# Optimization experiments

Measured on AMD Instinct MI355X. Metric: run time of the kernel, lower is better.

Reference implementation:

```python
import jax, jax.numpy as jnp
import numpy as np

N = 100000      # nodes
E = 1600000     # edges
F_IN = 64       # CFG.feature_dim
H = 128         # CFG.hidden_dim
G = 128         # graphs in batch
LN_EPS = 1e-5


def setup_inputs() -> dict:
    key = jax.random.key(0)
    ks = jax.random.split(key, 12)
    x = jax.random.normal(ks[0], (N, F_IN), dtype=jnp.float32)
    edge_index = jax.random.randint(ks[1], (2, E), 0, N)
    batch = jnp.sort(jax.random.randint(ks[2], (N,), 0, G))
    # GCNConv weights (glorot-ish scale) and biases
    W1 = jax.random.normal(ks[3], (F_IN, H), dtype=jnp.float32) * (1.0 / np.sqrt(F_IN))
    b1 = jnp.zeros((H,), jnp.float32)
    W2 = jax.random.normal(ks[4], (H, H), dtype=jnp.float32) * (1.0 / np.sqrt(H))
    b2 = jnp.zeros((H,), jnp.float32)
    # LayerNorm affine params
    g1 = jnp.ones((H,), jnp.float32)
    beta1 = jnp.zeros((H,), jnp.float32)
    g2 = jnp.ones((H,), jnp.float32)
    beta2 = jnp.zeros((H,), jnp.float32)
    return {"x": x, "edge_index": edge_index, "batch": batch,
            "W1": W1, "b1": b1, "g1": g1, "beta1": beta1,
            "W2": W2, "b2": b2, "g2": g2, "beta2": beta2,
            "num_graphs": G}


def _gcn_conv(h, W, b, src, dst, n):
    """PyG GCNConv: add self-loops, symmetric D^-1/2 (A+I) D^-1/2 (h W) + b."""
    hw = h @ W                                   # [n, out]
    loop = jnp.arange(n, dtype=src.dtype)
    s = jnp.concatenate([src, loop])             # [E+n]
    d = jnp.concatenate([dst, loop])
    deg = jax.ops.segment_sum(jnp.ones_like(s, jnp.float32), d, num_segments=n)
    dinv = jax.lax.rsqrt(jnp.maximum(deg, 1e-12))
    norm = dinv[s] * dinv[d]                     # [E+n]
    msg = hw[s] * norm[:, None]                  # gather + scale
    out = jax.ops.segment_sum(msg, d, num_segments=n)
    return out + b


def _layer_norm(h, gamma, beta):
    mu = jnp.mean(h, axis=-1, keepdims=True)
    var = jnp.mean(jnp.square(h - mu), axis=-1, keepdims=True)
    return (h - mu) * jax.lax.rsqrt(var + LN_EPS) * gamma + beta


def reference(x, edge_index, batch, W1, b1, g1, beta1, W2, b2, g2, beta2, num_graphs):
    src, dst = edge_index[0], edge_index[1]
    n = x.shape[0]
    h = _gcn_conv(x, W1, b1, src, dst, n)
    h = _layer_norm(h, g1, beta1)
    h = jax.nn.relu(h)
    h = _gcn_conv(h, W2, b2, src, dst, n)
    h = _layer_norm(h, g2, beta2)
    # is_inverted defaults to False -> no sign flip
    sums = jax.ops.segment_sum(h, batch, num_segments=num_graphs)      # [G, H]
    counts = jax.ops.segment_sum(jnp.ones((n,), jnp.float32), batch, num_segments=num_graphs)
    return sums / jnp.maximum(counts, 1.0)[:, None]
```

## Files before the change

### kernel.cpp

```cpp
#include <hip/hip_runtime.h>
#include <hip/hip_bf16.h>

#define LN_EPS 1e-5f

typedef __attribute__((ext_vector_type(8))) short short8v;
typedef __attribute__((ext_vector_type(4))) float float4v;

__device__ __forceinline__ float bflo(unsigned u) { return __uint_as_float(u << 16); }
__device__ __forceinline__ float bfhi(unsigned u) { return __uint_as_float(u & 0xffff0000u); }
__device__ __forceinline__ unsigned short f2bf(float f) {
    __hip_bfloat16 b = __float2bfloat16(f);
    return *reinterpret_cast<unsigned short*>(&b);
}
__device__ __forceinline__ unsigned pack2(float x, float y) {
    __hip_bfloat162 t = __float22bfloat162_rn(make_float2(x, y));
    return *reinterpret_cast<unsigned*>(&t);
}
__device__ __forceinline__ void add8(float* a, uint4 u) {
    a[0] += bflo(u.x); a[1] += bfhi(u.x);
    a[2] += bflo(u.y); a[3] += bfhi(u.y);
    a[4] += bflo(u.z); a[5] += bfhi(u.z);
    a[6] += bflo(u.w); a[7] += bfhi(u.w);
}

union U4S8 { uint4 u; short8v s; };


#define CHUNK 4096
#define NBMAX 512
#define BCAP 5120
#define CSRCAP 8192

__launch_bounds__(256)
__global__ void k_bucket(const int* __restrict__ src, const int* __restrict__ dst, int e,
                         int* __restrict__ gcnt, unsigned* __restrict__ stage) {
    __shared__ unsigned ebuf[CHUNK];
    __shared__ unsigned short ebkt[CHUNK];
    __shared__ int hist[NBMAX];
    __shared__ int base[NBMAX];
    int tid = threadIdx.x;
    int c0 = blockIdx.x * CHUNK;
    if (c0 >= e) return;
    int cnt = min(CHUNK, e - c0);

    for (int t = tid; t < NBMAX; t += 256) hist[t] = 0;
    __syncthreads();
    for (int t = tid; t < cnt; t += 256) {
        unsigned s = (unsigned)src[c0 + t];
        unsigned d = (unsigned)dst[c0 + t];
        ebuf[t] = s | ((d & 0xffu) << 24);
        ebkt[t] = (unsigned short)(d >> 8);
        atomicAdd(&hist[d >> 8], 1);
    }
    __syncthreads();
    for (int b = tid; b < NBMAX; b += 256) {
        int h = hist[b];
        if (h > 0) base[b] = b * BCAP + atomicAdd(&gcnt[b], h);
    }
    __syncthreads();
    for (int t = tid; t < cnt; t += 256) {
        int p = atomicAdd(&base[ebkt[t]], 1);
        stage[p] = ebuf[t];
    }
}

__launch_bounds__(256)
__global__ void k_csr(const unsigned* __restrict__ stage, const int* __restrict__ gcnt,
                      int* __restrict__ csr_src, int* __restrict__ row_start,
                      int* __restrict__ row_end, float* __restrict__ dinv,
                      const float* __restrict__ x, unsigned* __restrict__ xb, int n) {
    __shared__ int cntl[256];
    __shared__ int sc[256];
    __shared__ int excl[256];
    __shared__ float dfl[256];
    __shared__ int cbuf[CSRCAP];
    int b = blockIdx.x;
    int lo = b << 8;
    int nn = min(n - lo, 256);
    int tid = threadIdx.x;
    int s0 = b * BCAP;
    int cntB = gcnt[b];

    cntl[tid] = 0;
    __syncthreads();
    for (int t = tid; t < cntB; t += 256) {
        int dl = (int)(stage[s0 + t] >> 24);
        atomicAdd(&cntl[dl], 1);
    }
    __syncthreads();
    int deg = (tid < nn) ? cntl[tid] : 0;
    sc[tid] = deg; __syncthreads();
    for (int o = 1; o < 256; o <<= 1) {
        int t = (tid >= o) ? sc[tid - o] : 0;
        __syncthreads();
        sc[tid] += t;
        __syncthreads();
    }
    excl[tid] = sc[tid] - deg;
    float dv = rsqrtf((float)(deg + 1));
    dfl[tid] = dv;
    if (tid < nn) {
        row_start[lo + tid] = s0 + excl[tid];
        row_end[lo + tid]   = s0 + excl[tid] + deg;
        dinv[lo + tid] = dv;
    }
    cntl[tid] = 0;
    __syncthreads();
    for (int t = tid; t < cntB; t += 256) {
        unsigned ed = stage[s0 + t];
        int dl = (int)(ed >> 24);
        int r = atomicAdd(&cntl[dl], 1);
        int p = excl[dl] + r;
        if (p < CSRCAP) cbuf[p] = (int)(ed & 0x00ffffffu);
        else csr_src[s0 + p] = (int)(ed & 0x00ffffffu);
    }
    __syncthreads();
    int lim = min(cntB, CSRCAP);
    for (int t = tid; t < lim; t += 256) csr_src[s0 + t] = cbuf[t];

    const float4* x4 = (const float4*)x;
    uint2* xb2 = (uint2*)xb;
    for (int idx = tid; idx < nn * 16; idx += 256) {
        int node = idx >> 4, c = idx & 15;
        size_t p = ((size_t)(lo + node) << 4) + c;
        float4 v = x4[p];
        float d = dfl[node];
        xb2[p] = make_uint2(pack2(v.x * d, v.y * d), pack2(v.z * d, v.w * d));
    }
}


__global__ void k_agg64b(const uint4* __restrict__ x4, const float* __restrict__ dinv,
                         const int* __restrict__ row_start, const int* __restrict__ row_end,
                         const int* __restrict__ csr_src, uint4* __restrict__ out4, int n) {
    int lane = threadIdx.x & 63;
    int g = lane >> 3, c = lane & 7;
    int wid = (blockIdx.x * blockDim.x + threadIdx.x) >> 6;
    int nw = (gridDim.x * blockDim.x) >> 6;
    for (int i = wid; i < n; i += nw) {
        float a[8] = {0.f, 0.f, 0.f, 0.f, 0.f, 0.f, 0.f, 0.f};
        if (g == 0) {
            uint4 su = x4[(size_t)i * 8 + c];
            add8(a, su);
        }
        int j0 = row_start[i], j1 = row_end[i];
        int j = j0 + g;
        for (; j + 8 < j1; j += 16) {
            int s0 = csr_src[j], s1 = csr_src[j + 8];
            uint4 u0 = x4[(size_t)s0 * 8 + c];
            uint4 u1 = x4[(size_t)s1 * 8 + c];
            add8(a, u0);
            add8(a, u1);
        }
        if (j < j1) {
            int s0 = csr_src[j];
            uint4 u0 = x4[(size_t)s0 * 8 + c];
            add8(a, u0);
        }
        #pragma unroll
        for (int k = 0; k < 8; ++k) {
            a[k] += __shfl_xor(a[k], 8);
            a[k] += __shfl_xor(a[k], 16);
            a[k] += __shfl_xor(a[k], 32);
        }
        if (g == 0) {
            float di = dinv[i];
            uint4 o;
            o.x = pack2(a[0] * di, a[1] * di);
            o.y = pack2(a[2] * di, a[3] * di);
            o.z = pack2(a[4] * di, a[5] * di);
            o.w = pack2(a[6] * di, a[7] * di);
            out4[(size_t)i * 8 + c] = o;
        }
    }
}

__global__ void k_agg128b(const uint4* __restrict__ h4, const float* __restrict__ dinv,
                          const int* __restrict__ row_start, const int* __restrict__ row_end,
                          const int* __restrict__ csr_src, uint4* __restrict__ out4, int n) {
    int lane = threadIdx.x & 63;
    int q = lane >> 4, c = lane & 15;
    int wid = (blockIdx.x * blockDim.x + threadIdx.x) >> 6;
    int nw = (gridDim.x * blockDim.x) >> 6;
    for (int i = wid; i < n; i += nw) {
        float a[8] = {0.f, 0.f, 0.f, 0.f, 0.f, 0.f, 0.f, 0.f};
        if (q == 0) {
            uint4 su = h4[(size_t)i * 16 + c];
            add8(a, su);
        }
        int j0 = row_start[i], j1 = row_end[i];
        int j = j0 + q;
        for (; j + 12 < j1; j += 16) {
            int s0 = csr_src[j], s1 = csr_src[j + 4];
            int s2 = csr_src[j + 8], s3 = csr_src[j + 12];
            uint4 u0 = h4[(size_t)s0 * 16 + c];
            uint4 u1 = h4[(size_t)s1 * 16 + c];
            uint4 u2 = h4[(size_t)s2 * 16 + c];
            uint4 u3 = h4[(size_t)s3 * 16 + c];
            add8(a, u0);
            add8(a, u1);
            add8(a, u2);
            add8(a, u3);
        }
        for (; j < j1; j += 4) {
            int s0 = csr_src[j];
            uint4 u0 = h4[(size_t)s0 * 16 + c];
            add8(a, u0);
        }
        #pragma unroll
        for (int k = 0; k < 8; ++k) {
            a[k] += __shfl_xor(a[k], 16);
            a[k] += __shfl_xor(a[k], 32);
        }
        if (q == 0) {
            float di = dinv[i];
            uint4 o;
            o.x = pack2(a[0] * di, a[1] * di);
            o.y = pack2(a[2] * di, a[3] * di);
            o.z = pack2(a[4] * di, a[5] * di);
            o.w = pack2(a[6] * di, a[7] * di);
            out4[(size_t)i * 16 + c] = o;
        }
    }
}


__launch_bounds__(256)
__global__ void k_mm1(const unsigned* __restrict__ aggb, const float* __restrict__ W1,
                      const float* __restrict__ b1, const float* __restrict__ g1,
                      const float* __restrict__ be1, const float* __restrict__ dinv,
                      uint4* __restrict__ hb4, int ntiles) {
    int lane = threadIdx.x & 63;
    int wv = threadIdx.x >> 6;
    int wpb = blockDim.x >> 6;
    int lc = lane & 15, lg = lane >> 4;

    short8v B[2][8];
    #pragma unroll
    for (int ks = 0; ks < 2; ++ks)
        #pragma unroll
        for (int cb = 0; cb < 8; ++cb) {
            short8v f;
            #pragma unroll
            for (int j = 0; j < 8; ++j) {
                int k = ks * 32 + lg * 8 + j;
                f[j] = (short)f2bf(W1[k * 128 + cb * 16 + lc]);
            }
            B[ks][cb] = f;
        }
    float bs[8], gm[8], bt[8];
    #pragma unroll
    for (int cb = 0; cb < 8; ++cb) {
        bs[cb] = b1[cb * 16 + lc];
        gm[cb] = g1[cb * 16 + lc];
        bt[cb] = be1[cb * 16 + lc];
    }

    for (int t = blockIdx.x * wpb + wv; t < ntiles; t += gridDim.x * wpb) {
        size_t arow = (size_t)(t * 16 + lc) * 32;
        U4S8 a0, a1;
        a0.u = *(const uint4*)&aggb[arow + lg * 4];
        a1.u = *(const uint4*)&aggb[arow + 16 + lg * 4];
        float4v acc[8];
        #pragma unroll
        for (int cb = 0; cb < 8; ++cb) acc[cb] = (float4v){0.f, 0.f, 0.f, 0.f};
        #pragma unroll
        for (int cb = 0; cb < 8; ++cb) {
            acc[cb] = __builtin_amdgcn_mfma_f32_16x16x32_bf16(a0.s, B[0][cb], acc[cb], 0, 0, 0);
            acc[cb] = __builtin_amdgcn_mfma_f32_16x16x32_bf16(a1.s, B[1][cb], acc[cb], 0, 0, 0);
        }
        #pragma unroll
        for (int reg = 0; reg < 4; ++reg) {
            float s = 0.f, q = 0.f;
            #pragma unroll
            for (int cb = 0; cb < 8; ++cb) {
                float v = acc[cb][reg] + bs[cb];
                acc[cb][reg] = v;
                s += v; q = fmaf(v, v, q);
            }
            s += __shfl_xor(s, 1); q += __shfl_xor(q, 1);
            s += __shfl_xor(s, 2); q += __shfl_xor(q, 2);
            s += __shfl_xor(s, 4); q += __shfl_xor(q, 4);
            s += __shfl_xor(s, 8); q += __shfl_xor(q, 8);
            float mu = s * (1.f / 128.f);
            float var = fmaf(q, 1.f / 128.f, -mu * mu);
            float rstd = rsqrtf(var + LN_EPS);
            int rowi = t * 16 + lg * 4 + reg;
            float di = dinv[rowi];
            float o[8];
            #pragma unroll
            for (int cb = 0; cb < 8; ++cb)
                o[cb] = fmaxf(fmaf((acc[cb][reg] - mu) * rstd, gm[cb], bt[cb]), 0.f) * di;
            uint4 st;
            st.x = pack2(o[0], o[1]);
            st.y = pack2(o[2], o[3]);
            st.z = pack2(o[4], o[5]);
            st.w = pack2(o[6], o[7]);
            hb4[(size_t)rowi * 16 + lc] = st;
        }
    }
}

__launch_bounds__(256)
__global__ void k_mm2p(const unsigned* __restrict__ aggb, const float* __restrict__ W2,
                       const float* __restrict__ b2, const float* __restrict__ g2,
                       const float* __restrict__ be2, const int* __restrict__ batch,
                       float* __restrict__ psum, int ntiles, int n) {
    __shared__ uint4 sB[4 * 8 * 64];
    for (int idx = threadIdx.x; idx < 2048; idx += blockDim.x) {
        int l = idx & 63;
        int f = idx >> 6;
        int ks = f >> 3, cb = f & 7;
        int lg = l >> 4;
        int col = cb * 16 + (l & 15);
        float p[8];
        #pragma unroll
        for (int j = 0; j < 8; ++j)
            p[j] = W2[(j * 16 + ks * 4 + lg) * 128 + col];
        uint4 v;
        v.x = pack2(p[0], p[1]); v.y = pack2(p[2], p[3]);
        v.z = pack2(p[4], p[5]); v.w = pack2(p[6], p[7]);
        sB[idx] = v;
    }
    __syncthreads();

    int lane = threadIdx.x & 63;
    int wv = threadIdx.x >> 6;
    int wpb = blockDim.x >> 6;
    int lc = lane & 15, lg = lane >> 4;
    float bs[8], gm[8], bt[8];
    #pragma unroll
    for (int cb = 0; cb < 8; ++cb) {
        bs[cb] = b2[cb * 16 + lc];
        gm[cb] = g2[cb * 16 + lc];
        bt[cb] = be2[cb * 16 + lc];
    }

    for (int t = blockIdx.x * wpb + wv; t < ntiles; t += gridDim.x * wpb) {
        int row0 = t * 16;
        size_t arow = (size_t)(row0 + lc) * 64;
        U4S8 a[4];
        #pragma unroll
        for (int ks = 0; ks < 4; ++ks)
            a[ks].u = *(const uint4*)&aggb[arow + ks * 16 + lg * 4];
        float4v acc[8];
        #pragma unroll
        for (int cb = 0; cb < 8; ++cb) acc[cb] = (float4v){0.f, 0.f, 0.f, 0.f};
        #pragma unroll
        for (int ks = 0; ks < 4; ++ks) {
            #pragma unroll
            for (int cb = 0; cb < 8; ++cb) {
                U4S8 fb;
                fb.u = sB[(ks * 8 + cb) * 64 + lane];
                acc[cb] = __builtin_amdgcn_mfma_f32_16x16x32_bf16(a[ks].s, fb.s, acc[cb], 0, 0, 0);
            }
        }
        #pragma unroll
        for (int reg = 0; reg < 4; ++reg) {
            float s = 0.f, q = 0.f;
            #pragma unroll
            for (int cb = 0; cb < 8; ++cb) {
                float v = acc[cb][reg] + bs[cb];
                acc[cb][reg] = v;
                s += v; q = fmaf(v, v, q);
            }
            s += __shfl_xor(s, 1); q += __shfl_xor(q, 1);
            s += __shfl_xor(s, 2); q += __shfl_xor(q, 2);
            s += __shfl_xor(s, 4); q += __shfl_xor(q, 4);
            s += __shfl_xor(s, 8); q += __shfl_xor(q, 8);
            float mu = s * (1.f / 128.f);
            float var = fmaf(q, 1.f / 128.f, -mu * mu);
            float rstd = rsqrtf(var + LN_EPS);
            #pragma unroll
            for (int cb = 0; cb < 8; ++cb)
                acc[cb][reg] = fmaf((acc[cb][reg] - mu) * rstd, gm[cb], bt[cb]);
        }
        int gmin = batch[row0];
        int gmax = batch[row0 + 15];
        int rg[4];
        #pragma unroll
        for (int reg = 0; reg < 4; ++reg) rg[reg] = batch[row0 + lg * 4 + reg];
        for (int g = gmin; g <= gmax; ++g) {
            int lo = 0, hi = n;
            while (lo < hi) { int m = (lo + hi) >> 1; if (batch[m] < g) lo = m + 1; else hi = m; }
            int st = lo;
            hi = n;
            while (lo < hi) { int m = (lo + hi) >> 1; if (batch[m] < g + 1) lo = m + 1; else hi = m; }
            float rc = 1.f / fmaxf((float)(lo - st), 1.f);
            #pragma unroll
            for (int cb = 0; cb < 8; ++cb) {
                float s = 0.f;
                #pragma unroll
                for (int reg = 0; reg < 4; ++reg)
                    s += (rg[reg] == g) ? acc[cb][reg] : 0.f;
                s += __shfl_xor(s, 16);
                s += __shfl_xor(s, 32);
                if (lg == 0) atomicAdd(&psum[g * 128 + cb * 16 + lc], s * rc);
            }
        }
    }
}


extern "C" void kernel_launch(void* const* d_in, const int* in_sizes, int n_in,
                              void* d_out, int out_size, void* d_ws, size_t ws_size,
                              hipStream_t stream) {
    const float* x   = (const float*)d_in[0];
    const int*   ei  = (const int*)d_in[1];
    const int*   bat = (const int*)d_in[2];
    const float* W1  = (const float*)d_in[3];
    const float* b1  = (const float*)d_in[4];
    const float* g1  = (const float*)d_in[5];
    const float* be1 = (const float*)d_in[6];
    const float* W2  = (const float*)d_in[7];
    const float* b2  = (const float*)d_in[8];
    const float* g2  = (const float*)d_in[9];
    const float* be2 = (const float*)d_in[10];

    int n = in_sizes[0] / 64;
    int e = in_sizes[1] / 2;
    const int* src = ei;
    const int* dst = ei + e;

    int nbuckets = (n + 255) / 256;

    char* ws = (char*)d_ws;
    size_t off = 0;
    auto take = [&](size_t bytes) -> void* {
        void* p = ws + off;
        off = (off + bytes + 255) & ~(size_t)255;
        return p;
    };
    float*    dinv      = (float*)   take((size_t)n * 4);
    int*      row_start = (int*)     take((size_t)n * 4);
    int*      row_end   = (int*)     take((size_t)n * 4);
    int*      gcnt      = (int*)     take(NBMAX * 4);
    unsigned* stage     = (unsigned*)take((size_t)nbuckets * BCAP * 4);
    int*      csr_src   = (int*)     take((size_t)nbuckets * BCAP * 4);
    unsigned* xb        = (unsigned*)take((size_t)n * 64 * 2);
    unsigned* aggb      = (unsigned*)take((size_t)n * 64 * 2);
    unsigned* hb        = (unsigned*)take((size_t)n * 128 * 2);
    unsigned* agg2b     = (unsigned*)take((size_t)n * 128 * 2);

    hipMemsetAsync(gcnt, 0, NBMAX * 4, stream);
    hipMemsetAsync(d_out, 0, (size_t)out_size * 4, stream);

    int nbk = (e + CHUNK - 1) / CHUNK;
    k_bucket<<<nbk, 256, 0, stream>>>(src, dst, e, gcnt, stage);
    k_csr<<<nbuckets, 256, 0, stream>>>(stage, gcnt, csr_src, row_start, row_end,
                                        dinv, x, xb, n);

    k_agg64b<<<2048, 256, 0, stream>>>((const uint4*)xb, dinv, row_start, row_end,
                                       csr_src, (uint4*)aggb, n);

    int ntiles = n / 16;
    k_mm1<<<626, 256, 0, stream>>>(aggb, W1, b1, g1, be1, dinv,
                                   (uint4*)hb, ntiles);

    k_agg128b<<<2048, 256, 0, stream>>>((const uint4*)hb, dinv, row_start, row_end,
                                        csr_src, (uint4*)agg2b, n);

    k_mm2p<<<626, 256, 0, stream>>>(agg2b, W2, b2, g2, be2, bat,
                                    (float*)d_out, ntiles, n);
}
```

Baseline: 220.7 us.

## Precompute graph count reciprocals, stage W1 in LDS, drop LDS CSR buffer

Adds a tiny kernel that computes the per-graph reciprocal node counts once, replacing the two binary searches over the batch array that every tile in the second matmul kernel repeated for each graph. k_mm1 now converts W1 to bf16 once per block into shared memory, and each wave loads its fragments from there instead of doing 64 strided global loads per lane. k_csr writes CSR sources straight to global memory instead of staging them in a 32KB LDS buffer, which lowers LDS use and may raise occupancy at the cost of scattered global writes. The extra kernel launch adds a little fixed overhead.

Measured after the change: 215.5 us, median of 2. 1.02x faster.

```diff
diff --git a/kernel.cpp b/kernel.cpp
--- a/kernel.cpp
+++ b/kernel.cpp
@@ -8,10 +8,6 @@
 
 __device__ __forceinline__ float bflo(unsigned u) { return __uint_as_float(u << 16); }
 __device__ __forceinline__ float bfhi(unsigned u) { return __uint_as_float(u & 0xffff0000u); }
-__device__ __forceinline__ unsigned short f2bf(float f) {
-    __hip_bfloat16 b = __float2bfloat16(f);
-    return *reinterpret_cast<unsigned short*>(&b);
-}
 __device__ __forceinline__ unsigned pack2(float x, float y) {
     __hip_bfloat162 t = __float22bfloat162_rn(make_float2(x, y));
     return *reinterpret_cast<unsigned*>(&t);
@@ -29,7 +25,6 @@
 #define CHUNK 4096
 #define NBMAX 512
 #define BCAP 5120
-#define CSRCAP 8192
 
 __launch_bounds__(256)
 __global__ void k_bucket(const int* __restrict__ src, const int* __restrict__ dst, int e,
@@ -73,7 +68,6 @@
     __shared__ int sc[256];
     __shared__ int excl[256];
     __shared__ float dfl[256];
-    __shared__ int cbuf[CSRCAP];
     int b = blockIdx.x;
     int lo = b << 8;
     int nn = min(n - lo, 256);
@@ -110,13 +104,8 @@
         unsigned ed = stage[s0 + t];
         int dl = (int)(ed >> 24);
         int r = atomicAdd(&cntl[dl], 1);
-        int p = excl[dl] + r;
-        if (p < CSRCAP) cbuf[p] = (int)(ed & 0x00ffffffu);
-        else csr_src[s0 + p] = (int)(ed & 0x00ffffffu);
-    }
-    __syncthreads();
-    int lim = min(cntB, CSRCAP);
-    for (int t = tid; t < lim; t += 256) csr_src[s0 + t] = cbuf[t];
+        csr_src[s0 + excl[dl] + r] = (int)(ed & 0x00ffffffu);
+    }
 
     const float4* x4 = (const float4*)x;
     uint2* xb2 = (uint2*)xb;
@@ -127,6 +116,16 @@
         float d = dfl[node];
         xb2[p] = make_uint2(pack2(v.x * d, v.y * d), pack2(v.z * d, v.w * d));
     }
+}
+
+__global__ void k_rc(const int* __restrict__ batch, int n, float* __restrict__ rc) {
+    int g = threadIdx.x;
+    int lo = 0, hi = n;
+    while (lo < hi) { int m = (lo + hi) >> 1; if (batch[m] < g) lo = m + 1; else hi = m; }
+    int st = lo;
+    hi = n;
+    while (lo < hi) { int m = (lo + hi) >> 1; if (batch[m] < g + 1) lo = m + 1; else hi = m; }
+    rc[g] = 1.f / fmaxf((float)(lo - st), 1.f);
 }
 
 
@@ -230,24 +229,35 @@
                       const float* __restrict__ b1, const float* __restrict__ g1,
                       const float* __restrict__ be1, const float* __restrict__ dinv,
                       uint4* __restrict__ hb4, int ntiles) {
+    __shared__ uint4 sB[2 * 8 * 64];
+    for (int idx = threadIdx.x; idx < 1024; idx += blockDim.x) {
+        int l = idx & 63;
+        int f = idx >> 6;
+        int ks = f >> 3, cb = f & 7;
+        int kb = ks * 32 + (l >> 4) * 8;
+        int col = cb * 16 + (l & 15);
+        float p[8];
+        #pragma unroll
+        for (int j = 0; j < 8; ++j) p[j] = W1[(kb + j) * 128 + col];
+        uint4 v;
+        v.x = pack2(p[0], p[1]); v.y = pack2(p[2], p[3]);
+        v.z = pack2(p[4], p[5]); v.w = pack2(p[6], p[7]);
+        sB[idx] = v;
+    }
+    __syncthreads();
+
     int lane = threadIdx.x & 63;
     int wv = threadIdx.x >> 6;
     int wpb = blockDim.x >> 6;
     int lc = lane & 15, lg = lane >> 4;
 
-    short8v B[2][8];
+    U4S8 B[2][8];
     #pragma unroll
     for (int ks = 0; ks < 2; ++ks)
         #pragma unroll
-        for (int cb = 0; cb < 8; ++cb) {
-            short8v f;
-            #pragma unroll
-            for (int j = 0; j < 8; ++j) {
-                int k = ks * 32 + lg * 8 + j;
-                f[j] = (short)f2bf(W1[k * 128 + cb * 16 + lc]);
-            }
-            B[ks][cb] = f;
-        }
+        for (int cb = 0; cb < 8; ++cb)
+            B[ks][cb].u = sB[(ks * 8 + cb) * 64 + lane];
+
     float bs[8], gm[8], bt[8];
     #pragma unroll
     for (int cb = 0; cb < 8; ++cb) {
@@ -266,8 +276,8 @@
         for (int cb = 0; cb < 8; ++cb) acc[cb] = (float4v){0.f, 0.f, 0.f, 0.f};
         #pragma unroll
         for (int cb = 0; cb < 8; ++cb) {
-            acc[cb] = __builtin_amdgcn_mfma_f32_16x16x32_bf16(a0.s, B[0][cb], acc[cb], 0, 0, 0);
-            acc[cb] = __builtin_amdgcn_mfma_f32_16x16x32_bf16(a1.s, B[1][cb], acc[cb], 0, 0, 0);
+            acc[cb] = __builtin_amdgcn_mfma_f32_16x16x32_bf16(a0.s, B[0][cb].s, acc[cb], 0, 0, 0);
+            acc[cb] = __builtin_amdgcn_mfma_f32_16x16x32_bf16(a1.s, B[1][cb].s, acc[cb], 0, 0, 0);
         }
         #pragma unroll
         for (int reg = 0; reg < 4; ++reg) {
@@ -305,7 +315,7 @@
 __global__ void k_mm2p(const unsigned* __restrict__ aggb, const float* __restrict__ W2,
                        const float* __restrict__ b2, const float* __restrict__ g2,
                        const float* __restrict__ be2, const int* __restrict__ batch,
-                       float* __restrict__ psum, int ntiles, int n) {
+                       const float* __restrict__ rc, float* __restrict__ psum, int ntiles) {
     __shared__ uint4 sB[4 * 8 * 64];
     for (int idx = threadIdx.x; idx < 2048; idx += blockDim.x) {
         int l = idx & 63;
@@ -381,12 +391,7 @@
         #pragma unroll
         for (int reg = 0; reg < 4; ++reg) rg[reg] = batch[row0 + lg * 4 + reg];
         for (int g = gmin; g <= gmax; ++g) {
-            int lo = 0, hi = n;
-            while (lo < hi) { int m = (lo + hi) >> 1; if (batch[m] < g) lo = m + 1; else hi = m; }
-            int st = lo;
-            hi = n;
-            while (lo < hi) { int m = (lo + hi) >> 1; if (batch[m] < g + 1) lo = m + 1; else hi = m; }
-            float rc = 1.f / fmaxf((float)(lo - st), 1.f);
+            float rcg = rc[g];
             #pragma unroll
             for (int cb = 0; cb < 8; ++cb) {
                 float s = 0.f;
@@ -395,7 +400,7 @@
                     s += (rg[reg] == g) ? acc[cb][reg] : 0.f;
                 s += __shfl_xor(s, 16);
                 s += __shfl_xor(s, 32);
-                if (lg == 0) atomicAdd(&psum[g * 128 + cb * 16 + lc], s * rc);
+                if (lg == 0) atomicAdd(&psum[g * 128 + cb * 16 + lc], s * rcg);
             }
         }
     }
@@ -419,6 +424,7 @@
 
     int n = in_sizes[0] / 64;
     int e = in_sizes[1] / 2;
+    int G = out_size / 128;
     const int* src = ei;
     const int* dst = ei + e;
 
@@ -435,6 +441,7 @@
     int*      row_start = (int*)     take((size_t)n * 4);
     int*      row_end   = (int*)     take((size_t)n * 4);
     int*      gcnt      = (int*)     take(NBMAX * 4);
+    float*    rcbuf     = (float*)   take((size_t)G * 4);
     unsigned* stage     = (unsigned*)take((size_t)nbuckets * BCAP * 4);
     int*      csr_src   = (int*)     take((size_t)nbuckets * BCAP * 4);
     unsigned* xb        = (unsigned*)take((size_t)n * 64 * 2);
@@ -449,6 +456,7 @@
     k_bucket<<<nbk, 256, 0, stream>>>(src, dst, e, gcnt, stage);
     k_csr<<<nbuckets, 256, 0, stream>>>(stage, gcnt, csr_src, row_start, row_end,
                                         dinv, x, xb, n);
+    k_rc<<<1, G, 0, stream>>>(bat, n, rcbuf);
 
     k_agg64b<<<2048, 256, 0, stream>>>((const uint4*)xb, dinv, row_start, row_end,
                                        csr_src, (uint4*)aggb, n);
@@ -460,6 +468,6 @@
     k_agg128b<<<2048, 256, 0, stream>>>((const uint4*)hb, dinv, row_start, row_end,
                                         csr_src, (uint4*)agg2b, n);
 
-    k_mm2p<<<626, 256, 0, stream>>>(agg2b, W2, b2, g2, be2, bat,
-                                    (float*)d_out, ntiles, n);
-}
+    k_mm2p<<<626, 256, 0, stream>>>(agg2b, W2, b2, g2, be2, bat, rcbuf,
+                                    (float*)d_out, ntiles);
+}
```
